# Kernel optimization log

Measured on AMD Instinct MI355X. Metric: run time of the kernel, lower is better.

## Reference

```python
import jax, jax.numpy as jnp
import numpy as np

K_PROPOSALS = 16  # Marsaglia-Tsang acceptance rate > 0.95 for alpha > 1/3; P(all 16 rejected) < 1e-20

B, D_IN, H, L = 32768, 1024, 512, 64


def _glorot(key, shape):
    fan_in, fan_out = shape
    return jax.random.normal(key, shape, jnp.float32) * jnp.sqrt(2.0 / (fan_in + fan_out))


def setup_inputs() -> dict:
    key = jax.random.key(0)
    ks = jax.random.split(key, 4)
    return {
        "x": jax.random.normal(ks[0], (B, D_IN), jnp.float32),
        "W0": _glorot(ks[1], (D_IN, H)),
        "b0": jnp.zeros((H,), jnp.float32),
        "W1": _glorot(ks[2], (H, H)),
        "b1": jnp.zeros((H,), jnp.float32),
        "Wl": _glorot(ks[3], (H, L)),
        "bl": jnp.zeros((L,), jnp.float32),
    }


def _marsaglia_tsang_sample(alpha):
    """Vectorized Marsaglia-Tsang gamma(alpha, 1) rejection sampler.
    Draws K_PROPOSALS candidates per element and selects the first accepted one
    (equivalent to the original per-element while-loop, flattened for SIMD)."""
    d = alpha - 1.0 / 3.0                     # [B, L]
    c = 1.0 / jnp.sqrt(9.0 * d)               # [B, L]
    kz, ku = jax.random.split(jax.random.key(1))
    z = jax.random.normal(kz, (K_PROPOSALS,) + alpha.shape, alpha.dtype)   # [K, B, L]
    u = jax.random.uniform(ku, (K_PROPOSALS,) + alpha.shape, alpha.dtype,
                           minval=1e-7, maxval=1.0)                        # [K, B, L]
    v = (1.0 + c * z) ** 3                    # [K, B, L]
    pos = v > 0.0                             # equivalent to z > -1/c (= b1)
    safe_v = jnp.where(pos, v, 1.0)
    # accept iff z > b1 AND log(u) <= b2 (negation of the resampling condition)
    b2 = 0.5 * jnp.square(z) + d - d * safe_v + d * jnp.log(safe_v)
    accept = pos & (jnp.log(u) < b2)          # [K, B, L]
    first = jnp.argmax(accept, axis=0)        # index of first accepted proposal
    samples = d * safe_v                      # [K, B, L]
    return jnp.take_along_axis(samples, first[None], axis=0)[0]  # [B, L]


def reference(x, W0, b0, W1, b1, Wl, bl):
    # dense encoder: two ReLU hidden layers + linear latent head producing alpha
    h = jax.nn.relu(x @ W0 + b0)
    h = jax.nn.relu(h @ W1 + b1)
    # softplus + 0.5 keeps alpha > 1/3 so d > 0 (required by Marsaglia-Tsang)
    alpha = jax.nn.softplus(h @ Wl + bl) + 0.5
    sample = _marsaglia_tsang_sample(alpha)
    return alpha, sample
```

## Files before the change

kernel.cpp:

```cpp
#include <hip/hip_runtime.h>
#include <cstdint>
#include <cstddef>

typedef __attribute__((ext_vector_type(8))) short short8;
typedef __attribute__((ext_vector_type(4))) float floatx4;

constexpr int MDIM = 32768;
constexpr int DIN  = 1024;
constexpr int HDIM = 512;
constexpr int LDIM = 64;
constexpr uint32_t BL = (uint32_t)MDIM * (uint32_t)LDIM;

__host__ __device__ __forceinline__ void tf2x32(uint32_t k0, uint32_t k1,
                                                uint32_t x0, uint32_t x1,
                                                uint32_t& o0, uint32_t& o1) {
  const uint32_t k2 = k0 ^ k1 ^ 0x1BD11BDAu;
  x0 += k0; x1 += k1;
#define TFR(r) { x0 += x1; x1 = (x1 << (r)) | (x1 >> (32 - (r))); x1 ^= x0; }
  TFR(13) TFR(15) TFR(26) TFR(6)
  x0 += k1; x1 += k2 + 1u;
  TFR(17) TFR(29) TFR(16) TFR(24)
  x0 += k2; x1 += k0 + 2u;
  TFR(13) TFR(15) TFR(26) TFR(6)
  x0 += k0; x1 += k1 + 3u;
  TFR(17) TFR(29) TFR(16) TFR(24)
  x0 += k1; x1 += k2 + 4u;
  TFR(13) TFR(15) TFR(26) TFR(6)
  x0 += k2; x1 += k0 + 5u;
#undef TFR
  o0 = x0; o1 = x1;
}

__device__ __forceinline__ uint32_t tf_bits(uint32_t k0, uint32_t k1, uint32_t j) {
  uint32_t o0, o1;
  tf2x32(k0, k1, 0u, j, o0, o1);
  return o0 ^ o1;
}

__device__ __forceinline__ float b2f(unsigned short s) {
  return __uint_as_float((uint32_t)s << 16);
}
__device__ __forceinline__ unsigned short f2b(float f) {
  uint32_t u = __float_as_uint(f);
  u += 0x7fffu + ((u >> 16) & 1u);
  return (unsigned short)(u >> 16);
}
__device__ __forceinline__ void split3(float x, unsigned short& h,
                                       unsigned short& l, unsigned short& l2) {
  h = f2b(x);
  const float r = __fsub_rn(x, b2f(h));
  l = f2b(r);
  const float r2 = __fsub_rn(r, b2f(l));
  l2 = f2b(r2);
}

__device__ __forceinline__ float erfinv_f32(float x) {
  const float xx = __fmul_rn(x, x);
  float w = -log1pf(-xx);
  float p;
  if (w < 5.0f) {
    w = __fadd_rn(w, -2.5f);
    p = 2.81022636e-08f;
    p = __fadd_rn(__fmul_rn(p, w), 3.43273939e-07f);
    p = __fadd_rn(__fmul_rn(p, w), -3.5233877e-06f);
    p = __fadd_rn(__fmul_rn(p, w), -4.39150654e-06f);
    p = __fadd_rn(__fmul_rn(p, w), 0.00021858087f);
    p = __fadd_rn(__fmul_rn(p, w), -0.00125372503f);
    p = __fadd_rn(__fmul_rn(p, w), -0.00417768164f);
    p = __fadd_rn(__fmul_rn(p, w), 0.246640727f);
    p = __fadd_rn(__fmul_rn(p, w), 1.50140941f);
  } else {
    w = __fadd_rn(sqrtf(w), -3.0f);
    p = -0.000200214257f;
    p = __fadd_rn(__fmul_rn(p, w), 0.000100950558f);
    p = __fadd_rn(__fmul_rn(p, w), 0.00134934322f);
    p = __fadd_rn(__fmul_rn(p, w), -0.00367342844f);
    p = __fadd_rn(__fmul_rn(p, w), 0.00573950773f);
    p = __fadd_rn(__fmul_rn(p, w), -0.0076224613f);
    p = __fadd_rn(__fmul_rn(p, w), 0.00943887047f);
    p = __fadd_rn(__fmul_rn(p, w), 1.00167406f);
    p = __fadd_rn(__fmul_rn(p, w), 2.83297682f);
  }
  return __fmul_rn(p, x);
}

#define LO_N  (-0x1.fffffep-1f)
#define DIFF_N (2.0f)
#define SQRT2_F ((float)1.4142135623730951)
#define DIFF_U (0x1.fffffcp-1f)
#define MINV_U (1e-7f)
#define THIRD_F ((float)(1.0 / 3.0))

__device__ float gamma_sample(float alpha, uint32_t e,
                              uint32_t kz0, uint32_t kz1,
                              uint32_t ku0, uint32_t ku1) {
  const float d = __fsub_rn(alpha, THIRD_F);
  const float c = __fdiv_rn(1.0f, sqrtf(__fmul_rn(9.0f, d)));
  float samp0 = 0.0f;
#pragma unroll 1
  for (int k = 0; k < 16; ++k) {
    const uint32_t j = (uint32_t)k * BL + e;
    const uint32_t zb = tf_bits(kz0, kz1, j);
    const uint32_t ub = tf_bits(ku0, ku1, j);
    const float fz = __fsub_rn(__uint_as_float((zb >> 9) | 0x3f800000u), 1.0f);
    float un = __fadd_rn(__fmul_rn(fz, DIFF_N), LO_N);
    un = fmaxf(un, LO_N);
    const float z = __fmul_rn(SQRT2_F, erfinv_f32(un));
    const float fu = __fsub_rn(__uint_as_float((ub >> 9) | 0x3f800000u), 1.0f);
    float uu = __fadd_rn(__fmul_rn(fu, DIFF_U), MINV_U);
    uu = fmaxf(uu, MINV_U);
    const float t1 = __fadd_rn(1.0f, __fmul_rn(c, z));
    const float v = __fmul_rn(t1, __fmul_rn(t1, t1));
    const bool pos = (v > 0.0f);
    const float sv = pos ? v : 1.0f;
    const float b2 = __fadd_rn(
        __fsub_rn(__fadd_rn(__fmul_rn(0.5f, __fmul_rn(z, z)), d),
                  __fmul_rn(d, sv)),
        __fmul_rn(d, logf(sv)));
    const float lu = logf(uu);
    const float s = __fmul_rn(d, sv);
    if (k == 0) samp0 = s;
    if (pos && (lu < b2)) return s;
  }
  return samp0;
}

__global__ __launch_bounds__(256) void split_transpose(
    const float* __restrict__ W, unsigned short* __restrict__ D, int K, int N) {
  __shared__ unsigned short th[32][33], tl[32][33], tl2[32][33];
  const int t = threadIdx.x;
  const int nb = N / 32;
  const int k0 = (blockIdx.x / nb) * 32, n0 = (blockIdx.x % nb) * 32;
#pragma unroll
  for (int i = 0; i < 4; ++i) {
    const int e = i * 256 + t;
    const int kk = e >> 5, nn = e & 31;
    const float x = W[(size_t)(k0 + kk) * N + (n0 + nn)];
    split3(x, th[kk][nn], tl[kk][nn], tl2[kk][nn]);
  }
  __syncthreads();
  const size_t PL = (size_t)N * K;
#pragma unroll
  for (int i = 0; i < 4; ++i) {
    const int e = i * 256 + t;
    const int nn = e >> 5, kk = e & 31;
    const size_t o = (size_t)(n0 + nn) * K + (k0 + kk);
    D[o] = th[kk][nn];
    D[PL + o] = tl[kk][nn];
    D[2 * PL + o] = tl2[kk][nn];
  }
}

template <int K>
__global__ __launch_bounds__(256) void gemm_split_mfma(
    const float* __restrict__ A, const unsigned short* __restrict__ BT,
    const float* __restrict__ bias, float* __restrict__ C) {
  constexpr int N = 512;
  constexpr size_t PL = (size_t)N * K;
  __shared__ unsigned short As[3][128 * 32];
  __shared__ unsigned short Bs[3][128 * 32];
  const int t = threadIdx.x;
  const int lane = t & 63, w = t >> 6;
  const int wm = w >> 1, wn = w & 1;
  const int ln = lane & 15, kq = lane >> 4;
  const int bm = blockIdx.y * 128, bn = blockIdx.x * 128;

  floatx4 acc[4][4];
#pragma unroll
  for (int i = 0; i < 4; ++i)
#pragma unroll
    for (int j = 0; j < 4; ++j) acc[i][j] = (floatx4)0.0f;

  for (int k0 = 0; k0 < K; k0 += 32) {
#pragma unroll
    for (int p = 0; p < 3; ++p)
#pragma unroll
      for (int i = 0; i < 2; ++i) {
        const int e = w * 1024 + i * 512 + lane * 8;
        const int n = e >> 5, kc = e & 31;
        const unsigned short* g = BT + p * PL + (size_t)(bn + n) * K + (k0 + kc);
        __builtin_amdgcn_global_load_lds(
            (const __attribute__((address_space(1))) unsigned int*)g,
            (__attribute__((address_space(3))) unsigned int*)&Bs[p][w * 1024 + i * 512],
            16, 0, 0);
      }
#pragma unroll
    for (int it = 0; it < 4; ++it) {
      const int e4 = (it * 256 + t) * 4;
      const int m = e4 >> 5, kc = e4 & 31;
      const float4 q = *reinterpret_cast<const float4*>(
          &A[(size_t)(bm + m) * K + (k0 + kc)]);
      ushort4 h, l, l2;
      split3(q.x, h.x, l.x, l2.x);
      split3(q.y, h.y, l.y, l2.y);
      split3(q.z, h.z, l.z, l2.z);
      split3(q.w, h.w, l.w, l2.w);
      *reinterpret_cast<ushort4*>(&As[0][m * 32 + kc]) = h;
      *reinterpret_cast<ushort4*>(&As[1][m * 32 + kc]) = l;
      *reinterpret_cast<ushort4*>(&As[2][m * 32 + kc]) = l2;
    }
    __syncthreads();
    short8 af[3][4], bf[3][4];
#pragma unroll
    for (int mi = 0; mi < 4; ++mi)
#pragma unroll
      for (int p = 0; p < 3; ++p)
        af[p][mi] = *reinterpret_cast<const short8*>(
            &As[p][(wm * 64 + mi * 16 + ln) * 32 + kq * 8]);
#pragma unroll
    for (int ni = 0; ni < 4; ++ni)
#pragma unroll
      for (int p = 0; p < 3; ++p)
        bf[p][ni] = *reinterpret_cast<const short8*>(
            &Bs[p][(wn * 64 + ni * 16 + ln) * 32 + kq * 8]);
#pragma unroll
    for (int mi = 0; mi < 4; ++mi)
#pragma unroll
      for (int ni = 0; ni < 4; ++ni) {
        floatx4 a = acc[mi][ni];
        a = __builtin_amdgcn_mfma_f32_16x16x32_bf16(af[0][mi], bf[0][ni], a, 0, 0, 0);
        a = __builtin_amdgcn_mfma_f32_16x16x32_bf16(af[0][mi], bf[1][ni], a, 0, 0, 0);
        a = __builtin_amdgcn_mfma_f32_16x16x32_bf16(af[1][mi], bf[0][ni], a, 0, 0, 0);
        a = __builtin_amdgcn_mfma_f32_16x16x32_bf16(af[1][mi], bf[1][ni], a, 0, 0, 0);
        a = __builtin_amdgcn_mfma_f32_16x16x32_bf16(af[0][mi], bf[2][ni], a, 0, 0, 0);
        a = __builtin_amdgcn_mfma_f32_16x16x32_bf16(af[2][mi], bf[0][ni], a, 0, 0, 0);
        acc[mi][ni] = a;
      }
    __syncthreads();
  }
#pragma unroll
  for (int ni = 0; ni < 4; ++ni) {
    const int n = bn + wn * 64 + ni * 16 + ln;
    const float bb = bias[n];
#pragma unroll
    for (int mi = 0; mi < 4; ++mi)
#pragma unroll
      for (int r = 0; r < 4; ++r) {
        const int m = bm + wm * 64 + mi * 16 + kq * 4 + r;
        C[(size_t)m * N + n] = fmaxf(__fadd_rn(acc[mi][ni][r], bb), 0.0f);
      }
  }
}

__global__ __launch_bounds__(256) void gemm3_sampler(
    const float* __restrict__ A, const float* __restrict__ Wl,
    const float* __restrict__ bl, float* __restrict__ out,
    uint32_t kz0, uint32_t kz1, uint32_t ku0, uint32_t ku1) {
  constexpr int BM = 64, BK = 16, K = 512, N = 64;
  constexpr int LDA = BM + 4, LDB = N + 4;
  __shared__ float Ash[BK * LDA];
  __shared__ float Bsh[BK * LDB];
  const int t = threadIdx.x;
  const int tx = t % 16, ty = t / 16;
  const int bm = blockIdx.x * BM;
  float acc[4][4] = {};
  const int aRow = t / 4, aCol = (t % 4) * 4;
  const int bRow = t / 16, bCol = (t % 16) * 4;

  for (int k0 = 0; k0 < K; k0 += BK) {
    {
      const float4 q = *reinterpret_cast<const float4*>(
          A + (size_t)(bm + aRow) * K + (k0 + aCol));
      Ash[(aCol + 0) * LDA + aRow] = q.x;
      Ash[(aCol + 1) * LDA + aRow] = q.y;
      Ash[(aCol + 2) * LDA + aRow] = q.z;
      Ash[(aCol + 3) * LDA + aRow] = q.w;
    }
    {
      const float4 q = *reinterpret_cast<const float4*>(
          Wl + (size_t)(k0 + bRow) * N + bCol);
      *reinterpret_cast<float4*>(&Bsh[bRow * LDB + bCol]) = q;
    }
    __syncthreads();
#pragma unroll
    for (int k = 0; k < BK; ++k) {
      float a[4], b[4];
#pragma unroll
      for (int i = 0; i < 4; ++i) a[i] = Ash[k * LDA + ty * 4 + i];
#pragma unroll
      for (int j = 0; j < 4; ++j) b[j] = Bsh[k * LDB + tx * 4 + j];
#pragma unroll
      for (int i = 0; i < 4; ++i)
#pragma unroll
        for (int j = 0; j < 4; ++j) acc[i][j] = fmaf(a[i], b[j], acc[i][j]);
    }
    __syncthreads();
  }

  float bv[4];
#pragma unroll
  for (int j = 0; j < 4; ++j) bv[j] = bl[tx * 4 + j];

  for (int i = 0; i < 4; ++i) {
    const int row = bm + ty * 4 + i;
    float av[4], sv4[4];
    for (int j = 0; j < 4; ++j) {
      const float x = __fadd_rn(acc[i][j], bv[j]);
      const float sp = __fadd_rn(fmaxf(x, 0.0f), log1pf(expf(-fabsf(x))));
      const float alpha = __fadd_rn(sp, 0.5f);
      const uint32_t e = (uint32_t)row * 64u + (uint32_t)(tx * 4 + j);
      const float s = gamma_sample(alpha, e, kz0, kz1, ku0, ku1);
      av[j] = alpha;
      sv4[j] = s;
    }
    *reinterpret_cast<float4*>(&out[(size_t)row * 64 + tx * 4]) =
        *reinterpret_cast<float4*>(av);
    *reinterpret_cast<float4*>(&out[(size_t)BL + (size_t)row * 64 + tx * 4]) =
        *reinterpret_cast<float4*>(sv4);
  }
}

extern "C" void kernel_launch(void* const* d_in, const int* in_sizes, int n_in,
                              void* d_out, int out_size, void* d_ws, size_t ws_size,
                              hipStream_t stream) {
  (void)in_sizes; (void)n_in; (void)out_size; (void)ws_size;
  const float* x  = (const float*)d_in[0];
  const float* W0 = (const float*)d_in[1];
  const float* b0 = (const float*)d_in[2];
  const float* W1 = (const float*)d_in[3];
  const float* b1 = (const float*)d_in[4];
  const float* Wl = (const float*)d_in[5];
  const float* bl = (const float*)d_in[6];
  float* h1 = (float*)d_ws;
  float* h2 = h1 + (size_t)MDIM * HDIM;
  float* out = (float*)d_out;

  unsigned short* W0T = (unsigned short*)out;
  unsigned short* W1T = (unsigned short*)(out + BL);

  uint32_t kz0, kz1, ku0, ku1;
  tf2x32(0u, 1u, 0u, 0u, kz0, kz1);
  tf2x32(0u, 1u, 0u, 1u, ku0, ku1);

  split_transpose<<<dim3((DIN / 32) * (HDIM / 32)), 256, 0, stream>>>(
      W0, W0T, DIN, HDIM);
  split_transpose<<<dim3((HDIM / 32) * (HDIM / 32)), 256, 0, stream>>>(
      W1, W1T, HDIM, HDIM);

  dim3 g12(HDIM / 128, MDIM / 128);
  gemm_split_mfma<DIN><<<g12, 256, 0, stream>>>(x, W0T, b0, h1);
  gemm_split_mfma<HDIM><<<g12, 256, 0, stream>>>(h1, W1T, b1, h2);
  gemm3_sampler<<<dim3(MDIM / 64), 256, 0, stream>>>(h2, Wl, bl, out,
                                                     kz0, kz1, ku0, ku1);
}
```

Before: 528.9 us.

## Compact gamma rejections into shared queue and remap GEMM blocks per XCD

The sampler now draws only the first proposal for every element and pushes rejected elements into a shared-memory queue. A second pass redistributes those elements across all threads for the remaining proposals, which cuts wavefront divergence in the rejection loop. The two MFMA GEMMs also switch to a 1D grid with an XCD-aware block mapping so that blocks sharing rows of A run on the same XCD for L2 reuse. This adds 24KB of LDS in the sampler, which may reduce occupancy.

```diff
diff --git a/kernel.cpp b/kernel.cpp
--- a/kernel.cpp
+++ b/kernel.cpp
@@ -91,38 +91,30 @@
 #define MINV_U (1e-7f)
 #define THIRD_F ((float)(1.0 / 3.0))
 
-__device__ float gamma_sample(float alpha, uint32_t e,
-                              uint32_t kz0, uint32_t kz1,
-                              uint32_t ku0, uint32_t ku1) {
-  const float d = __fsub_rn(alpha, THIRD_F);
-  const float c = __fdiv_rn(1.0f, sqrtf(__fmul_rn(9.0f, d)));
-  float samp0 = 0.0f;
-#pragma unroll 1
-  for (int k = 0; k < 16; ++k) {
-    const uint32_t j = (uint32_t)k * BL + e;
-    const uint32_t zb = tf_bits(kz0, kz1, j);
-    const uint32_t ub = tf_bits(ku0, ku1, j);
-    const float fz = __fsub_rn(__uint_as_float((zb >> 9) | 0x3f800000u), 1.0f);
-    float un = __fadd_rn(__fmul_rn(fz, DIFF_N), LO_N);
-    un = fmaxf(un, LO_N);
-    const float z = __fmul_rn(SQRT2_F, erfinv_f32(un));
-    const float fu = __fsub_rn(__uint_as_float((ub >> 9) | 0x3f800000u), 1.0f);
-    float uu = __fadd_rn(__fmul_rn(fu, DIFF_U), MINV_U);
-    uu = fmaxf(uu, MINV_U);
-    const float t1 = __fadd_rn(1.0f, __fmul_rn(c, z));
-    const float v = __fmul_rn(t1, __fmul_rn(t1, t1));
-    const bool pos = (v > 0.0f);
-    const float sv = pos ? v : 1.0f;
-    const float b2 = __fadd_rn(
-        __fsub_rn(__fadd_rn(__fmul_rn(0.5f, __fmul_rn(z, z)), d),
-                  __fmul_rn(d, sv)),
-        __fmul_rn(d, logf(sv)));
-    const float lu = logf(uu);
-    const float s = __fmul_rn(d, sv);
-    if (k == 0) samp0 = s;
-    if (pos && (lu < b2)) return s;
-  }
-  return samp0;
+__device__ __forceinline__ float gamma_draw(float d, float c, uint32_t j,
+                                            uint32_t kz0, uint32_t kz1,
+                                            uint32_t ku0, uint32_t ku1,
+                                            bool& accept) {
+  const uint32_t zb = tf_bits(kz0, kz1, j);
+  const uint32_t ub = tf_bits(ku0, ku1, j);
+  const float fz = __fsub_rn(__uint_as_float((zb >> 9) | 0x3f800000u), 1.0f);
+  float un = __fadd_rn(__fmul_rn(fz, DIFF_N), LO_N);
+  un = fmaxf(un, LO_N);
+  const float z = __fmul_rn(SQRT2_F, erfinv_f32(un));
+  const float fu = __fsub_rn(__uint_as_float((ub >> 9) | 0x3f800000u), 1.0f);
+  float uu = __fadd_rn(__fmul_rn(fu, DIFF_U), MINV_U);
+  uu = fmaxf(uu, MINV_U);
+  const float t1 = __fadd_rn(1.0f, __fmul_rn(c, z));
+  const float v = __fmul_rn(t1, __fmul_rn(t1, t1));
+  const bool pos = (v > 0.0f);
+  const float sv = pos ? v : 1.0f;
+  const float b2 = __fadd_rn(
+      __fsub_rn(__fadd_rn(__fmul_rn(0.5f, __fmul_rn(z, z)), d),
+                __fmul_rn(d, sv)),
+      __fmul_rn(d, logf(sv)));
+  const float lu = logf(uu);
+  accept = pos && (lu < b2);
+  return __fmul_rn(d, sv);
 }
 
 __global__ __launch_bounds__(256) void split_transpose(
@@ -163,7 +155,10 @@
   const int lane = t & 63, w = t >> 6;
   const int wm = w >> 1, wn = w & 1;
   const int ln = lane & 15, kq = lane >> 4;
-  const int bm = blockIdx.y * 128, bn = blockIdx.x * 128;
+  const int b = blockIdx.x;
+  const int xcd = b & 7, slot = b >> 3;
+  const int bm = (xcd * 32 + (slot >> 2)) * 128;
+  const int bn = (slot & 3) * 128;
 
   floatx4 acc[4][4];
 #pragma unroll
@@ -250,9 +245,13 @@
   constexpr int LDA = BM + 4, LDB = N + 4;
   __shared__ float Ash[BK * LDA];
   __shared__ float Bsh[BK * LDB];
+  __shared__ float alphaS[BM * N];
+  __shared__ unsigned short queue[BM * N];
+  __shared__ int nrej;
   const int t = threadIdx.x;
   const int tx = t % 16, ty = t / 16;
   const int bm = blockIdx.x * BM;
+  if (t == 0) nrej = 0;
   float acc[4][4] = {};
   const int aRow = t / 4, aCol = (t % 4) * 4;
   const int bRow = t / 16, bCol = (t % 16) * 4;
@@ -291,22 +290,56 @@
 #pragma unroll
   for (int j = 0; j < 4; ++j) bv[j] = bl[tx * 4 + j];
 
+#pragma unroll 1
   for (int i = 0; i < 4; ++i) {
     const int row = bm + ty * 4 + i;
     float av[4], sv4[4];
+    unsigned short rejloc[4];
+    int nrl = 0;
+#pragma unroll 1
     for (int j = 0; j < 4; ++j) {
       const float x = __fadd_rn(acc[i][j], bv[j]);
       const float sp = __fadd_rn(fmaxf(x, 0.0f), log1pf(expf(-fabsf(x))));
       const float alpha = __fadd_rn(sp, 0.5f);
-      const uint32_t e = (uint32_t)row * 64u + (uint32_t)(tx * 4 + j);
-      const float s = gamma_sample(alpha, e, kz0, kz1, ku0, ku1);
+      const int le = (ty * 4 + i) * 64 + tx * 4 + j;
+      alphaS[le] = alpha;
+      const float d = __fsub_rn(alpha, THIRD_F);
+      const float c = __fdiv_rn(1.0f, sqrtf(__fmul_rn(9.0f, d)));
+      bool acc0;
+      const float s0 = gamma_draw(d, c, (uint32_t)row * 64u + (uint32_t)(tx * 4 + j),
+                                  kz0, kz1, ku0, ku1, acc0);
       av[j] = alpha;
-      sv4[j] = s;
+      sv4[j] = s0;
+      if (!acc0) rejloc[nrl++] = (unsigned short)le;
+    }
+    if (nrl) {
+      const int base = atomicAdd(&nrej, nrl);
+      for (int q = 0; q < nrl; ++q) queue[base + q] = rejloc[q];
     }
     *reinterpret_cast<float4*>(&out[(size_t)row * 64 + tx * 4]) =
         *reinterpret_cast<float4*>(av);
     *reinterpret_cast<float4*>(&out[(size_t)BL + (size_t)row * 64 + tx * 4]) =
         *reinterpret_cast<float4*>(sv4);
+  }
+  __syncthreads();
+
+  const int n = nrej;
+  for (int q = t; q < n; q += 256) {
+    const int le = queue[q];
+    const float alpha = alphaS[le];
+    const float d = __fsub_rn(alpha, THIRD_F);
+    const float c = __fdiv_rn(1.0f, sqrtf(__fmul_rn(9.0f, d)));
+    const uint32_t e = (uint32_t)bm * 64u + (uint32_t)le;
+#pragma unroll 1
+    for (int k = 1; k < 16; ++k) {
+      bool acck;
+      const float s = gamma_draw(d, c, (uint32_t)k * BL + e,
+                                 kz0, kz1, ku0, ku1, acck);
+      if (acck) {
+        out[(size_t)BL + e] = s;
+        break;
+      }
+    }
   }
 }
 
@@ -337,9 +370,8 @@
   split_transpose<<<dim3((HDIM / 32) * (HDIM / 32)), 256, 0, stream>>>(
       W1, W1T, HDIM, HDIM);
 
-  dim3 g12(HDIM / 128, MDIM / 128);
-  gemm_split_mfma<DIN><<<g12, 256, 0, stream>>>(x, W0T, b0, h1);
-  gemm_split_mfma<HDIM><<<g12, 256, 0, stream>>>(h1, W1T, b1, h2);
+  gemm_split_mfma<DIN><<<dim3(1024), 256, 0, stream>>>(x, W0T, b0, h1);
+  gemm_split_mfma<HDIM><<<dim3(1024), 256, 0, stream>>>(h1, W1T, b1, h2);
   gemm3_sampler<<<dim3(MDIM / 64), 256, 0, stream>>>(h2, Wl, bl, out,
                                                      kz0, kz1, ku0, ku1);
 }
```

Result: slower. 587.5 us (+11.1%).
